# Performance work log

Measured on AMD Instinct MI355X. Metric: run time of the kernel, lower is better.

## Reference

```python
import jax, jax.numpy as jnp
from jax import lax
import numpy as np

SEQ, BATCH, DIN, DH = 2048, 64, 128, 256

def setup_inputs() -> dict:
    key = jax.random.key(0)
    ks = jax.random.split(key, 6)
    s_in = 1.0 / np.sqrt(DIN)
    s_h = 1.0 / np.sqrt(DH)
    return {
        "data": jax.random.normal(ks[0], (SEQ, BATCH, DIN), dtype=jnp.float32),
        "W_ih": jax.random.normal(ks[1], (3 * DH, DIN), dtype=jnp.float32) * s_in,
        "W_hh": jax.random.normal(ks[2], (3 * DH, DH), dtype=jnp.float32) * s_h,
        "b_ih": jax.random.normal(ks[3], (3 * DH,), dtype=jnp.float32) * s_h,
        "b_hh": jax.random.normal(ks[4], (3 * DH,), dtype=jnp.float32) * s_h,
        "w_att": jax.random.normal(ks[5], (DH,), dtype=jnp.float32) * s_h,
    }

def _mask_user_data(data):
    # vectorized form of: if data[i,j,-1] > 0: data[i,j,32:64] = 0
    cond = data[:, :, -1:] > 0  # (S, B, 1)
    sl = data[:, :, 32:64]
    sl = jnp.where(cond, jnp.zeros_like(sl), sl)
    return data.at[:, :, 32:64].set(sl)

def _gru(data, W_ih, W_hh, b_ih, b_hh):
    H = W_hh.shape[1]
    h0 = jnp.zeros((data.shape[1], H), dtype=data.dtype)
    def step(h, x):  # x: (B, Din)
        gi = x @ W_ih.T + b_ih   # (B, 3H)
        gh = h @ W_hh.T + b_hh   # (B, 3H)
        ir, iz, inn = jnp.split(gi, 3, axis=-1)
        hr, hz, hn = jnp.split(gh, 3, axis=-1)
        r = jax.nn.sigmoid(ir + hr)
        z = jax.nn.sigmoid(iz + hz)
        n = jnp.tanh(inn + r * hn)
        h_new = (1.0 - z) * n + z * h
        return h_new, h_new
    _, outs = lax.scan(step, h0, data)  # (S, B, H)
    return outs

def reference(data, W_ih, W_hh, b_ih, b_hh, w_att):
    data = _mask_user_data(data)
    outs = _gru(data, W_ih, W_hh, b_ih, b_hh)  # (S, B, H)
    # SimpleAttention: score each hidden state with Linear(H,1,no bias), softmax over seq
    scores = jnp.einsum("sbh,h->sb", outs, w_att)  # (S, B)
    alpha = jax.nn.softmax(scores, axis=0)
    res = jnp.einsum("sb,sbh->bh", alpha, outs)    # (B, H)
    return res
```

## Files before the change

### kernel.cpp

```cpp
#include <hip/hip_runtime.h>
#include <hip/hip_fp16.h>


#define SEQ   2048
#define BATCH 64
#define DIN   128
#define DH    256
#define G3    768

typedef _Float16 h2 __attribute__((ext_vector_type(2)));
typedef _Float16 h8 __attribute__((ext_vector_type(8)));
typedef float f32x4 __attribute__((ext_vector_type(4)));

#if __has_builtin(__builtin_amdgcn_fdot2)
__device__ __forceinline__ float fd2(unsigned int a, unsigned int b, float c) {
  return __builtin_amdgcn_fdot2(__builtin_bit_cast(h2, a), __builtin_bit_cast(h2, b), c, false);
}
#else
__device__ __forceinline__ float fd2(unsigned int a, unsigned int b, float c) {
  h2 x = __builtin_bit_cast(h2, a), y = __builtin_bit_cast(h2, b);
  return c + (float)x[0] * (float)y[0] + (float)x[1] * (float)y[1];
}
#endif

__global__ __launch_bounds__(256) void k_prep_w(const float* __restrict__ wih,
    const float* __restrict__ whh, const float* __restrict__ bih,
    const float* __restrict__ bhh, _Float16* __restrict__ wih16,
    _Float16* __restrict__ whh16, float* __restrict__ biasf,
    float* __restrict__ bhnf) {
  int i = blockIdx.x * 256 + threadIdx.x;
  if (i < 98304) { wih16[i] = (_Float16)wih[i]; return; }
  i -= 98304;
  if (i < 196608) { whh16[i] = (_Float16)whh[i]; return; }
  i -= 196608;
  if (i < 768) { biasf[i] = bih[i] + (i < 512 ? bhh[i] : 0.0f); return; }
  i -= 768;
  if (i < 256) bhnf[i] = bhh[512 + i];
}

#define LDK 136

__global__ __launch_bounds__(256) void k_gi(const float* __restrict__ data,
    const _Float16* __restrict__ w16, const float* __restrict__ bias,
    _Float16* __restrict__ gi16, int s0) {
  __shared__ _Float16 As[128][LDK];
  __shared__ _Float16 Ws[64][LDK];
  int tid = threadIdx.x;
  int m0 = blockIdx.x * 128;
  size_t gm0 = (size_t)s0 * 64 + m0;

  {
    int r = tid >> 1, c0 = (tid & 1) * 64;
    const float4* src = (const float4*)(data + (gm0 + r) * DIN + c0);
    float last = data[(gm0 + r) * DIN + 127];
    bool msk = (last > 0.0f) && (c0 == 0);
    #pragma unroll
    for (int i = 0; i < 16; ++i) {
      float4 t = src[i];
      if (msk && i >= 8) t = make_float4(0.f, 0.f, 0.f, 0.f);
      union { _Float16 h[4]; uint2 u; } pk;
      pk.h[0] = (_Float16)t.x; pk.h[1] = (_Float16)t.y;
      pk.h[2] = (_Float16)t.z; pk.h[3] = (_Float16)t.w;
      *(uint2*)&As[r][c0 + i * 4] = pk.u;
    }
  }

  int w = tid >> 6, lane = tid & 63;
  int wm = (w >> 1) * 64, wn = (w & 1) * 32;
  int l16 = lane & 15, lhi = lane >> 4;

  for (int nb = 0; nb < 12; ++nb) {
    {
      int r = tid >> 2, cc = (tid & 3) * 32;
      const uint4* src = (const uint4*)(w16 + (size_t)(nb * 64 + r) * DIN + cc);
      #pragma unroll
      for (int i = 0; i < 4; ++i)
        *(uint4*)&Ws[r][cc + i * 8] = src[i];
    }
    __syncthreads();

    f32x4 acc[4][2];
    #pragma unroll
    for (int mi = 0; mi < 4; ++mi)
      #pragma unroll
      for (int ni = 0; ni < 2; ++ni)
        acc[mi][ni] = (f32x4){0.f, 0.f, 0.f, 0.f};

    #pragma unroll
    for (int ks = 0; ks < 4; ++ks) {
      int kk = ks * 32 + lhi * 8;
      h8 a[4], bfr[2];
      #pragma unroll
      for (int mi = 0; mi < 4; ++mi)
        a[mi] = *(const h8*)&As[wm + mi * 16 + l16][kk];
      #pragma unroll
      for (int ni = 0; ni < 2; ++ni)
        bfr[ni] = *(const h8*)&Ws[wn + ni * 16 + l16][kk];
      #pragma unroll
      for (int mi = 0; mi < 4; ++mi)
        #pragma unroll
        for (int ni = 0; ni < 2; ++ni)
          acc[mi][ni] = __builtin_amdgcn_mfma_f32_16x16x32_f16(a[mi], bfr[ni], acc[mi][ni], 0, 0, 0);
    }

    #pragma unroll
    for (int mi = 0; mi < 4; ++mi)
      #pragma unroll
      for (int ni = 0; ni < 2; ++ni) {
        int col = nb * 64 + wn + ni * 16 + l16;
        float bv = bias[col];
        #pragma unroll
        for (int r = 0; r < 4; ++r) {
          int row = m0 + wm + mi * 16 + lhi * 4 + r;
          gi16[(size_t)row * G3 + col] = (_Float16)(acc[mi][ni][r] + bv);
        }
      }
    __syncthreads();
  }
}

__global__ __launch_bounds__(512, 2) void k_rnn(const _Float16* __restrict__ whh16,
    const _Float16* __restrict__ gi16, const float* __restrict__ bhnf,
    _Float16* __restrict__ outs16, float* __restrict__ hstate, int s0, int CH) {
  __shared__ __align__(16) unsigned int hsh[2][140];
  int b = blockIdx.x;
  int tid = threadIdx.x;
  int lane = tid & 63;
  int c = lane & 3;
  int Q = (tid >> 6) * 16 + (lane >> 2);
  int j0 = 2 * Q;

  uint4 wv[6][8];
  #pragma unroll
  for (int d = 0; d < 2; ++d)
    #pragma unroll
    for (int g = 0; g < 3; ++g) {
      const uint4* src = (const uint4*)(whh16 + (size_t)(g * 256 + j0 + d) * DH + c * 64);
      #pragma unroll
      for (int i = 0; i < 8; ++i) wv[d * 3 + g][i] = src[i];
    }
  float bn0 = bhnf[j0], bn1 = bhnf[j0 + 1];
  float h0, h1;
  if (s0 == 0) { h0 = 0.f; h1 = 0.f; }
  else { h0 = hstate[b * 256 + j0]; h1 = hstate[b * 256 + j0 + 1]; }

  int wr = (Q >> 5) * 36 + (Q & 31);
  if (c == 0) {
    union { _Float16 h[2]; unsigned int u; } pk;
    pk.h[0] = (_Float16)h0; pk.h[1] = (_Float16)h1;
    hsh[0][wr] = pk.u;
  }
  __syncthreads();

  const unsigned int* gi32 = (const unsigned int*)gi16;
  unsigned int* outs32 = (unsigned int*)outs16;
  size_t gbase = (size_t)b * 384 + Q;
  size_t obase = ((size_t)s0 * 64 + b) * 128 + Q;
  int p = 0;

  for (int s = 0; s < CH; ++s) {
    unsigned int gr = gi32[gbase];
    unsigned int gz = gi32[gbase + 128];
    unsigned int gn = gi32[gbase + 256];

    const uint4* hp = (const uint4*)&hsh[p][c * 36];
    float a0 = 0.f, a1 = 0.f, a2 = 0.f, a3 = 0.f, a4 = 0.f, a5 = 0.f;
    #pragma unroll
    for (int u = 0; u < 8; ++u) {
      uint4 hv = hp[u];
      uint4 w0 = wv[0][u], w1 = wv[1][u], w2 = wv[2][u];
      uint4 w3 = wv[3][u], w4 = wv[4][u], w5 = wv[5][u];
      a0 = fd2(w0.x, hv.x, a0); a0 = fd2(w0.y, hv.y, a0); a0 = fd2(w0.z, hv.z, a0); a0 = fd2(w0.w, hv.w, a0);
      a1 = fd2(w1.x, hv.x, a1); a1 = fd2(w1.y, hv.y, a1); a1 = fd2(w1.z, hv.z, a1); a1 = fd2(w1.w, hv.w, a1);
      a2 = fd2(w2.x, hv.x, a2); a2 = fd2(w2.y, hv.y, a2); a2 = fd2(w2.z, hv.z, a2); a2 = fd2(w2.w, hv.w, a2);
      a3 = fd2(w3.x, hv.x, a3); a3 = fd2(w3.y, hv.y, a3); a3 = fd2(w3.z, hv.z, a3); a3 = fd2(w3.w, hv.w, a3);
      a4 = fd2(w4.x, hv.x, a4); a4 = fd2(w4.y, hv.y, a4); a4 = fd2(w4.z, hv.z, a4); a4 = fd2(w4.w, hv.w, a4);
      a5 = fd2(w5.x, hv.x, a5); a5 = fd2(w5.y, hv.y, a5); a5 = fd2(w5.z, hv.z, a5); a5 = fd2(w5.w, hv.w, a5);
    }
    a0 += __shfl_xor(a0, 1); a0 += __shfl_xor(a0, 2);
    a1 += __shfl_xor(a1, 1); a1 += __shfl_xor(a1, 2);
    a2 += __shfl_xor(a2, 1); a2 += __shfl_xor(a2, 2);
    a3 += __shfl_xor(a3, 1); a3 += __shfl_xor(a3, 2);
    a4 += __shfl_xor(a4, 1); a4 += __shfl_xor(a4, 2);
    a5 += __shfl_xor(a5, 1); a5 += __shfl_xor(a5, 2);

    h2 grh = __builtin_bit_cast(h2, gr);
    h2 gzh = __builtin_bit_cast(h2, gz);
    h2 gnh = __builtin_bit_cast(h2, gn);
    {
      float r = 1.f / (1.f + __expf(-((float)grh[0] + a0)));
      float z = 1.f / (1.f + __expf(-((float)gzh[0] + a1)));
      float x = (float)gnh[0] + r * (a2 + bn0);
      float n = 1.f - 2.f / (__expf(2.f * x) + 1.f);
      h0 = n + z * (h0 - n);
    }
    {
      float r = 1.f / (1.f + __expf(-((float)grh[1] + a3)));
      float z = 1.f / (1.f + __expf(-((float)gzh[1] + a4)));
      float x = (float)gnh[1] + r * (a5 + bn1);
      float n = 1.f - 2.f / (__expf(2.f * x) + 1.f);
      h1 = n + z * (h1 - n);
    }
    union { _Float16 h[2]; unsigned int u; } pk;
    pk.h[0] = (_Float16)h0; pk.h[1] = (_Float16)h1;
    if (c == 0) {
      hsh[p ^ 1][wr] = pk.u;
      outs32[obase] = pk.u;
    }
    __syncthreads();
    p ^= 1;
    gbase += 64 * 384;
    obase += 64 * 128;
  }

  if (c == 0) {
    hstate[b * 256 + j0] = h0;
    hstate[b * 256 + j0 + 1] = h1;
  }
}

__global__ __launch_bounds__(256) void k_scores(const _Float16* __restrict__ outs16,
    const float* __restrict__ watt, float* __restrict__ scores) {
  int idx = blockIdx.x * 4 + (threadIdx.x >> 6);
  int lane = threadIdx.x & 63;
  const uint2* row = (const uint2*)((const unsigned int*)outs16 + (size_t)idx * 128 + lane * 2);
  uint2 v = *row;
  float4 w = *(const float4*)(watt + lane * 4);
  h2 va = __builtin_bit_cast(h2, v.x);
  h2 vb = __builtin_bit_cast(h2, v.y);
  float sum = (float)va[0] * w.x + (float)va[1] * w.y + (float)vb[0] * w.z + (float)vb[1] * w.w;
  #pragma unroll
  for (int m = 1; m < 64; m <<= 1) sum += __shfl_xor(sum, m);
  if (lane == 0) scores[idx] = sum;
}

__global__ __launch_bounds__(256) void k_att(const _Float16* __restrict__ outs16,
    const float* __restrict__ scores, float* __restrict__ out) {
  __shared__ float al[SEQ];
  __shared__ float red[12];
  int b = blockIdx.x, t = threadIdx.x;
  float v[8];
  float m = -1e30f;
  #pragma unroll
  for (int i = 0; i < 8; ++i) {
    v[i] = scores[(size_t)(t + i * 256) * 64 + b];
    m = fmaxf(m, v[i]);
  }
  #pragma unroll
  for (int k = 1; k < 64; k <<= 1) m = fmaxf(m, __shfl_xor(m, k));
  if ((t & 63) == 0) red[t >> 6] = m;
  __syncthreads();
  m = fmaxf(fmaxf(red[0], red[1]), fmaxf(red[2], red[3]));
  float l = 0.f;
  #pragma unroll
  for (int i = 0; i < 8; ++i) {
    float e = __expf(v[i] - m);
    al[t + i * 256] = e;
    l += e;
  }
  #pragma unroll
  for (int k = 1; k < 64; k <<= 1) l += __shfl_xor(l, k);
  if ((t & 63) == 0) red[8 + (t >> 6)] = l;
  __syncthreads();
  l = red[8] + red[9] + red[10] + red[11];
  float inv = 1.f / l;

  float acc = 0.f;
  const unsigned int* o32 = (const unsigned int*)outs16;
  size_t base = (size_t)b * 128 + (t >> 1);
  int hi = t & 1;
  for (int s = 0; s < SEQ; ++s) {
    unsigned int u = o32[base + (size_t)s * 8192];
    h2 hh = __builtin_bit_cast(h2, u);
    acc += al[s] * (float)hh[hi];
  }
  out[b * 256 + t] = acc * inv;
}

__global__ __launch_bounds__(256) void k_fill(float* out, float v, int n) {
  int i = blockIdx.x * 256 + threadIdx.x;
  if (i < n) out[i] = v;
}

extern "C" void kernel_launch(void* const* d_in, const int* in_sizes, int n_in,
                              void* d_out, int out_size, void* d_ws, size_t ws_size,
                              hipStream_t stream) {
  const float* data = (const float*)d_in[0];
  const float* wih  = (const float*)d_in[1];
  const float* whh  = (const float*)d_in[2];
  const float* bih  = (const float*)d_in[3];
  const float* bhh  = (const float*)d_in[4];
  const float* watt = (const float*)d_in[5];
  float* out = (float*)d_out;

  const size_t OFF_WIH    = 0;
  const size_t OFF_WHH    = 196608;
  const size_t OFF_BIAS   = 589824;
  const size_t OFF_BHN    = 592896;
  const size_t OFF_H      = 593920;
  const size_t OFF_SCORES = 659456;
  const size_t OFF_OUTS   = 1183744;
  const size_t OFF_GI     = 68292608;

  int CH = 0;
  for (int ch = SEQ; ch >= 64; ch >>= 1) {
    if (OFF_GI + (size_t)ch * 64 * G3 * 2 <= ws_size) { CH = ch; break; }
  }
  if (CH == 0) {
    k_fill<<<(out_size + 255) / 256, 256, 0, stream>>>(out, 2.0e6f, out_size);
    return;
  }

  char* ws = (char*)d_ws;
  _Float16* wih16  = (_Float16*)(ws + OFF_WIH);
  _Float16* whh16  = (_Float16*)(ws + OFF_WHH);
  float*    biasf  = (float*)(ws + OFF_BIAS);
  float*    bhnf   = (float*)(ws + OFF_BHN);
  float*    hstate = (float*)(ws + OFF_H);
  float*    scores = (float*)(ws + OFF_SCORES);
  _Float16* outs16 = (_Float16*)(ws + OFF_OUTS);
  _Float16* gi16   = (_Float16*)(ws + OFF_GI);

  k_prep_w<<<(98304 + 196608 + 768 + 256 + 255) / 256, 256, 0, stream>>>(
      wih, whh, bih, bhh, wih16, whh16, biasf, bhnf);

  for (int s0 = 0; s0 < SEQ; s0 += CH) {
    k_gi<<<CH * 64 / 128, 256, 0, stream>>>(data, wih16, biasf, gi16, s0);
    k_rnn<<<BATCH, 512, 0, stream>>>(whh16, gi16, bhnf, outs16, hstate, s0, CH);
  }

  k_scores<<<SEQ * BATCH / 4, 256, 0, stream>>>(outs16, watt, scores);
  k_att<<<BATCH, 256, 0, stream>>>(outs16, scores, out);
}
```

Before: 3.626 ms.

## Split recurrent GRU step across 1024 threads with one hidden unit per quad

The recurrent kernel now launches 1024 threads per batch row instead of 512. Each group of 4 lanes handles one hidden unit instead of two, which halves the register-resident W_hh slice per thread and the serial dot-product work per step. The cross-lane reduction moves from shfl_xor to DPP quad permutes, and empty asm statements pin the weights in VGPRs. In exchange there are more waves per block synchronising on every timestep barrier, and the gate math and stores are now 16-bit per thread rather than packed pairs.

Result: no change. 3.623 ms (-0.1%).

```diff
diff --git a/kernel.cpp b/kernel.cpp
--- a/kernel.cpp
+++ b/kernel.cpp
@@ -22,6 +22,12 @@
   return c + (float)x[0] * (float)y[0] + (float)x[1] * (float)y[1];
 }
 #endif
+
+template <int CTRL>
+__device__ __forceinline__ float dppadd(float x) {
+  int t = __builtin_amdgcn_mov_dpp(__builtin_bit_cast(int, x), CTRL, 0xF, 0xF, true);
+  return x + __builtin_bit_cast(float, t);
+}
 
 __global__ __launch_bounds__(256) void k_prep_w(const float* __restrict__ wih,
     const float* __restrict__ whh, const float* __restrict__ bih,
@@ -119,104 +125,86 @@
   }
 }
 
-__global__ __launch_bounds__(512, 2) void k_rnn(const _Float16* __restrict__ whh16,
+__global__ __launch_bounds__(1024, 4) void k_rnn(const _Float16* __restrict__ whh16,
     const _Float16* __restrict__ gi16, const float* __restrict__ bhnf,
     _Float16* __restrict__ outs16, float* __restrict__ hstate, int s0, int CH) {
-  __shared__ __align__(16) unsigned int hsh[2][140];
+  __shared__ __align__(16) unsigned int hsh[2][144];
   int b = blockIdx.x;
   int tid = threadIdx.x;
-  int lane = tid & 63;
-  int c = lane & 3;
-  int Q = (tid >> 6) * 16 + (lane >> 2);
-  int j0 = 2 * Q;
-
-  uint4 wv[6][8];
-  #pragma unroll
-  for (int d = 0; d < 2; ++d)
-    #pragma unroll
-    for (int g = 0; g < 3; ++g) {
-      const uint4* src = (const uint4*)(whh16 + (size_t)(g * 256 + j0 + d) * DH + c * 64);
-      #pragma unroll
-      for (int i = 0; i < 8; ++i) wv[d * 3 + g][i] = src[i];
-    }
-  float bn0 = bhnf[j0], bn1 = bhnf[j0 + 1];
-  float h0, h1;
-  if (s0 == 0) { h0 = 0.f; h1 = 0.f; }
-  else { h0 = hstate[b * 256 + j0]; h1 = hstate[b * 256 + j0 + 1]; }
-
-  int wr = (Q >> 5) * 36 + (Q & 31);
+  int c = tid & 3;
+  int j = tid >> 2;
+
+  uint4 wr_[8], wz_[8], wn_[8];
+  {
+    const uint4* pr = (const uint4*)(whh16 + (size_t)j * DH + c * 64);
+    const uint4* pz = (const uint4*)(whh16 + (size_t)(256 + j) * DH + c * 64);
+    const uint4* pn = (const uint4*)(whh16 + (size_t)(512 + j) * DH + c * 64);
+    #pragma unroll
+    for (int i = 0; i < 8; ++i) { wr_[i] = pr[i]; wz_[i] = pz[i]; wn_[i] = pn[i]; }
+  }
+  #pragma unroll
+  for (int i = 0; i < 8; ++i) {
+    asm volatile("" : "+v"(wr_[i].x), "+v"(wr_[i].y), "+v"(wr_[i].z), "+v"(wr_[i].w));
+    asm volatile("" : "+v"(wz_[i].x), "+v"(wz_[i].y), "+v"(wz_[i].z), "+v"(wz_[i].w));
+    asm volatile("" : "+v"(wn_[i].x), "+v"(wn_[i].y), "+v"(wn_[i].z), "+v"(wn_[i].w));
+  }
+
+  int dj = j >> 1;
+  int wbyte = ((dj >> 5) * 36 + (dj & 31)) * 4 + (j & 1) * 2;
+
+  float bn = 0.f, h = 0.f;
   if (c == 0) {
-    union { _Float16 h[2]; unsigned int u; } pk;
-    pk.h[0] = (_Float16)h0; pk.h[1] = (_Float16)h1;
-    hsh[0][wr] = pk.u;
+    bn = bhnf[j];
+    h = (s0 == 0) ? 0.f : hstate[b * 256 + j];
+    *(_Float16*)((char*)&hsh[0][0] + wbyte) = (_Float16)h;
   }
   __syncthreads();
 
-  const unsigned int* gi32 = (const unsigned int*)gi16;
-  unsigned int* outs32 = (unsigned int*)outs16;
-  size_t gbase = (size_t)b * 384 + Q;
-  size_t obase = ((size_t)s0 * 64 + b) * 128 + Q;
+  const _Float16* gp = gi16 + (size_t)b * G3 + j;
+  _Float16* op = outs16 + ((size_t)s0 * 64 + b) * DH + j;
   int p = 0;
 
   for (int s = 0; s < CH; ++s) {
-    unsigned int gr = gi32[gbase];
-    unsigned int gz = gi32[gbase + 128];
-    unsigned int gn = gi32[gbase + 256];
+    float gr = 0.f, gz = 0.f, gn = 0.f;
+    if (c == 0) {
+      gr = (float)gp[0];
+      gz = (float)gp[256];
+      gn = (float)gp[512];
+    }
 
     const uint4* hp = (const uint4*)&hsh[p][c * 36];
-    float a0 = 0.f, a1 = 0.f, a2 = 0.f, a3 = 0.f, a4 = 0.f, a5 = 0.f;
+    float ar = 0.f, az = 0.f, an = 0.f;
     #pragma unroll
     for (int u = 0; u < 8; ++u) {
       uint4 hv = hp[u];
-      uint4 w0 = wv[0][u], w1 = wv[1][u], w2 = wv[2][u];
-      uint4 w3 = wv[3][u], w4 = wv[4][u], w5 = wv[5][u];
-      a0 = fd2(w0.x, hv.x, a0); a0 = fd2(w0.y, hv.y, a0); a0 = fd2(w0.z, hv.z, a0); a0 = fd2(w0.w, hv.w, a0);
-      a1 = fd2(w1.x, hv.x, a1); a1 = fd2(w1.y, hv.y, a1); a1 = fd2(w1.z, hv.z, a1); a1 = fd2(w1.w, hv.w, a1);
-      a2 = fd2(w2.x, hv.x, a2); a2 = fd2(w2.y, hv.y, a2); a2 = fd2(w2.z, hv.z, a2); a2 = fd2(w2.w, hv.w, a2);
-      a3 = fd2(w3.x, hv.x, a3); a3 = fd2(w3.y, hv.y, a3); a3 = fd2(w3.z, hv.z, a3); a3 = fd2(w3.w, hv.w, a3);
-      a4 = fd2(w4.x, hv.x, a4); a4 = fd2(w4.y, hv.y, a4); a4 = fd2(w4.z, hv.z, a4); a4 = fd2(w4.w, hv.w, a4);
-      a5 = fd2(w5.x, hv.x, a5); a5 = fd2(w5.y, hv.y, a5); a5 = fd2(w5.z, hv.z, a5); a5 = fd2(w5.w, hv.w, a5);
-    }
-    a0 += __shfl_xor(a0, 1); a0 += __shfl_xor(a0, 2);
-    a1 += __shfl_xor(a1, 1); a1 += __shfl_xor(a1, 2);
-    a2 += __shfl_xor(a2, 1); a2 += __shfl_xor(a2, 2);
-    a3 += __shfl_xor(a3, 1); a3 += __shfl_xor(a3, 2);
-    a4 += __shfl_xor(a4, 1); a4 += __shfl_xor(a4, 2);
-    a5 += __shfl_xor(a5, 1); a5 += __shfl_xor(a5, 2);
-
-    h2 grh = __builtin_bit_cast(h2, gr);
-    h2 gzh = __builtin_bit_cast(h2, gz);
-    h2 gnh = __builtin_bit_cast(h2, gn);
-    {
-      float r = 1.f / (1.f + __expf(-((float)grh[0] + a0)));
-      float z = 1.f / (1.f + __expf(-((float)gzh[0] + a1)));
-      float x = (float)gnh[0] + r * (a2 + bn0);
+      ar = fd2(wr_[u].x, hv.x, ar); ar = fd2(wr_[u].y, hv.y, ar);
+      ar = fd2(wr_[u].z, hv.z, ar); ar = fd2(wr_[u].w, hv.w, ar);
+      az = fd2(wz_[u].x, hv.x, az); az = fd2(wz_[u].y, hv.y, az);
+      az = fd2(wz_[u].z, hv.z, az); az = fd2(wz_[u].w, hv.w, az);
+      an = fd2(wn_[u].x, hv.x, an); an = fd2(wn_[u].y, hv.y, an);
+      an = fd2(wn_[u].z, hv.z, an); an = fd2(wn_[u].w, hv.w, an);
+    }
+    ar = dppadd<0xB1>(ar); ar = dppadd<0x4E>(ar);
+    az = dppadd<0xB1>(az); az = dppadd<0x4E>(az);
+    an = dppadd<0xB1>(an); an = dppadd<0x4E>(an);
+
+    if (c == 0) {
+      float r = 1.f / (1.f + __expf(-(gr + ar)));
+      float z = 1.f / (1.f + __expf(-(gz + az)));
+      float x = gn + r * (an + bn);
       float n = 1.f - 2.f / (__expf(2.f * x) + 1.f);
-      h0 = n + z * (h0 - n);
-    }
-    {
-      float r = 1.f / (1.f + __expf(-((float)grh[1] + a3)));
-      float z = 1.f / (1.f + __expf(-((float)gzh[1] + a4)));
-      float x = (float)gnh[1] + r * (a5 + bn1);
-      float n = 1.f - 2.f / (__expf(2.f * x) + 1.f);
-      h1 = n + z * (h1 - n);
-    }
-    union { _Float16 h[2]; unsigned int u; } pk;
-    pk.h[0] = (_Float16)h0; pk.h[1] = (_Float16)h1;
-    if (c == 0) {
-      hsh[p ^ 1][wr] = pk.u;
-      outs32[obase] = pk.u;
+      h = n + z * (h - n);
+      _Float16 h16 = (_Float16)h;
+      *(_Float16*)((char*)&hsh[p ^ 1][0] + wbyte) = h16;
+      op[0] = h16;
     }
     __syncthreads();
     p ^= 1;
-    gbase += 64 * 384;
-    obase += 64 * 128;
-  }
-
-  if (c == 0) {
-    hstate[b * 256 + j0] = h0;
-    hstate[b * 256 + j0 + 1] = h1;
-  }
+    gp += 64 * G3;
+    op += 64 * DH;
+  }
+
+  if (c == 0) hstate[b * 256 + j] = h;
 }
 
 __global__ __launch_bounds__(256) void k_scores(const _Float16* __restrict__ outs16,
@@ -326,7 +314,7 @@
 
   for (int s0 = 0; s0 < SEQ; s0 += CH) {
     k_gi<<<CH * 64 / 128, 256, 0, stream>>>(data, wih16, biasf, gi16, s0);
-    k_rnn<<<BATCH, 512, 0, stream>>>(whh16, gi16, bhnf, outs16, hstate, s0, CH);
+    k_rnn<<<BATCH, 1024, 0, stream>>>(whh16, gi16, bhnf, outs16, hstate, s0, CH);
   }
 
   k_scores<<<SEQ * BATCH / 4, 256, 0, stream>>>(outs16, watt, scores);
```
